# Optimization experiments

Measured on AMD Instinct MI355X. Metric: run time of the kernel, lower is better.

The kernel has to match this reference:

```python
import jax, jax.numpy as jnp
import numpy as np

B = 16384      # games
BS = 19        # board size
N2 = BS * BS   # 361
G = 8          # groups per board
S = 4          # stones per group
R = B * G      # total groups
K = R * S      # total stones
M = N2         # hash history length (H*W*history_factor)
I32MIN = np.iinfo(np.int32).min
I32MAX = np.iinfo(np.int32).max
NEG = jnp.float32(-1e9)


def setup_inputs() -> dict:
    key = jax.random.key(0)
    ks = jax.random.split(key, 10)
    logits = jax.random.normal(ks[0], (B, BS, BS), dtype=jnp.float32)
    legal_mask = jax.random.uniform(ks[1], (B, BS, BS)) < 0.7
    current_player = jax.random.randint(ks[2], (B,), 0, 2, dtype=jnp.int32)
    current_hash = jax.random.randint(ks[3], (B,), 0, I32MAX, dtype=jnp.int32)
    hash_history = jax.random.randint(ks[4], (B, M), 0, I32MAX, dtype=jnp.int32)
    move_count = jax.random.randint(ks[5], (B,), 0, M, dtype=jnp.int32)
    ZposT = jax.random.randint(ks[6], (3, N2), 0, I32MAX, dtype=jnp.int32)
    stone_global_index = jax.random.randint(ks[7], (K,), 0, N2, dtype=jnp.int32)
    stone_global_pointer = jnp.arange(R + 1, dtype=jnp.int32) * S          # CSR: stones per group
    group_global_pointer_per_board = jnp.arange(B + 1, dtype=jnp.int32) * G  # CSR: groups per board
    cap_idx = jax.random.randint(ks[8], (B, N2, 4), 0, G, dtype=jnp.int32)
    cap_on = jax.random.uniform(ks[9], (B, N2, 4)) < 0.05
    captured_group_local_index = jnp.where(cap_on, cap_idx, jnp.int32(-1))
    return {
        "logits": logits,
        "legal_mask": legal_mask,
        "current_player": current_player,
        "current_hash": current_hash,
        "hash_history": hash_history,
        "move_count": move_count,
        "ZposT": ZposT,
        "stone_global_index": stone_global_index,
        "stone_global_pointer": stone_global_pointer,
        "group_global_pointer_per_board": group_global_pointer_per_board,
        "captured_group_local_index": captured_group_local_index,
    }


def reference(logits, legal_mask, current_player, current_hash, hash_history,
              move_count, ZposT, stone_global_index, stone_global_pointer,
              group_global_pointer_per_board, captured_group_local_index):
    Bn, H, W = legal_mask.shape
    Rn = stone_global_pointer.shape[0] - 1
    Kn = stone_global_index.shape[0]
    z_empty, z_black, z_white = ZposT[0], ZposT[1], ZposT[2]

    # Placement delta: empty -> current player's stone, for every candidate point. (B, N2)
    placement_delta = z_empty[None, :] ^ jnp.where(
        (current_player == 0)[:, None], z_black[None, :], z_white[None, :])

    # Map each group -> board, each stone -> group (CSR expansion).
    groups_per_board = group_global_pointer_per_board[1:] - group_global_pointer_per_board[:-1]
    group_board = jnp.repeat(jnp.arange(Bn, dtype=jnp.int32), groups_per_board,
                             total_repeat_length=Rn)
    stones_per_group = stone_global_pointer[1:] - stone_global_pointer[:-1]
    group_for_stone = jnp.repeat(jnp.arange(Rn, dtype=jnp.int32), stones_per_group,
                                 total_repeat_length=Kn)
    stone_board = group_board[group_for_stone]

    # Per-stone removal delta: opponent stone -> empty.
    opp_for_stone = (1 - current_player)[stone_board]           # (K,)
    si = stone_global_index.astype(jnp.int32)
    z_opp = ZposT[1 + opp_for_stone, si]
    per_stone_delta = z_opp ^ z_empty[si]                        # (K,) int32

    # Segmented XOR reduction over each group's stones via XOR prefix scan.
    prefix = jax.lax.associative_scan(jnp.bitwise_xor, per_stone_delta)
    start = stone_global_pointer[:-1]
    end = stone_global_pointer[1:]
    end_val = prefix[jnp.clip(end - 1, 0)]
    start_val = jnp.where(start > 0, prefix[jnp.clip(start - 1, 0)], jnp.int32(0))
    group_xor = end_val ^ start_val                              # (R,) per-group removal delta

    # Gather capture deltas for up to 4 captured neighbor groups per candidate move.
    offs = group_global_pointer_per_board[:-1][:, None, None]    # (B,1,1)
    flat_ids = jnp.clip(captured_group_local_index, 0) + offs    # (B,N2,4)
    cap_vals = jnp.where(captured_group_local_index >= 0, group_xor[flat_ids], jnp.int32(0))
    capture_delta = cap_vals[..., 0] ^ cap_vals[..., 1] ^ cap_vals[..., 2] ^ cap_vals[..., 3]

    candidate = current_hash[:, None] ^ placement_delta ^ capture_delta  # (B, N2)

    # Super-ko repeat detection against hash history (mask, sort, searchsorted).
    Mh = hash_history.shape[1]
    valid = jnp.arange(Mh, dtype=jnp.int32)[None, :] < jnp.minimum(move_count, Mh)[:, None]
    masked_hist = jnp.where(valid, hash_history, jnp.int32(I32MIN))
    sorted_hist = jnp.sort(masked_hist, axis=1)
    idx = jnp.clip(
        jax.vmap(lambda h, c: jnp.searchsorted(h, c, side='right'))(sorted_hist, candidate) - 1,
        0)
    found = jnp.take_along_axis(sorted_hist, idx, axis=1)
    repeat = (found == candidate).reshape(Bn, H, W)

    final_mask = legal_mask & ~repeat
    return jnp.where(final_mask, logits, NEG)
```

## Files before the change

kernel.cpp:

```cpp
#include <hip/hip_runtime.h>
#include <stdint.h>

#define N2 361
#define BMW 1024u
#define EMPTY 0x80000000u
#define NEGV -998244352.0f

__global__ __launch_bounds__(256, 4) void go_repeat_mask_kernel(
    const float* __restrict__ logits,
    const void*  __restrict__ legal_raw,
    const int*   __restrict__ current_player,
    const int*   __restrict__ current_hash,
    const int*   __restrict__ hash_history,
    const int*   __restrict__ move_count,
    const int*   __restrict__ ZposT,
    const int*   __restrict__ stone_global_index,
    const int*   __restrict__ stone_global_pointer,
    const int*   __restrict__ group_global_pointer,
    const int4*  __restrict__ captured4,
    float*       __restrict__ out,
    int packed_bits)
{
    __shared__ unsigned s_bm[4 * BMW];

    const int tid  = threadIdx.x;
    const int wid  = tid >> 6;
    const int lane = tid & 63;
    const int b    = __builtin_amdgcn_readfirstlane(blockIdx.x * 4 + wid);
    unsigned* bm   = s_bm + wid * BMW;
    const size_t bbase = (size_t)b * N2;

    const int      cp  = current_player[b];
    const unsigned ch  = (unsigned)current_hash[b];
    int            cnt = move_count[b];
    cnt = cnt < 0 ? 0 : (cnt > N2 ? N2 : cnt);

    const int*  hist  = hash_history + bbase;
    const int4* hist4 = (const int4*)hist;
    const int4  ha    = hist4[lane];
    const int4  hb    = (lane < 26) ? hist4[64 + lane] : int4{0,0,0,0};
    const int   hc    = (lane == 26) ? hist[360] : 0;

    const unsigned* lwd = (const unsigned*)legal_raw;
    const unsigned dv0 = lwd[lane];
    const unsigned dv1 = (lane < 27) ? lwd[64 + lane] : 0u;

    int sp0 = 0, sp1 = 0;
    const int g0 = group_global_pointer[b];
    const int g1 = group_global_pointer[b + 1];
    if (lane < 32) {
        const int r = g0 + (lane >> 2);
        if (r < g1) { sp0 = stone_global_pointer[r]; sp1 = stone_global_pointer[r + 1]; }
    }

    int4  cap[6];
    float lg[6];
    unsigned zz[6];
    const int prow = (1 + cp) * N2;
    #pragma unroll
    for (int s = 0; s < 6; ++s) {
        const int n  = lane + 64 * s;
        const int nc = (n < N2) ? n : (N2 - 1);
        const size_t q = bbase + nc;
        cap[s] = captured4[q];
        lg[s]  = logits[q];
        zz[s]  = (unsigned)ZposT[nc] ^ (unsigned)ZposT[prow + nc];
    }

    auto classify = [](unsigned v) -> unsigned {
        unsigned f = 0;
        #pragma unroll
        for (int j = 0; j < 4; ++j) {
            const unsigned bv = (v >> (8 * j)) & 0xFFu;
            if (bv > 1u) f |= 1u;
            if (j != 0 && bv != 0u) f |= 2u;
        }
        const unsigned x = v & 0xFFFFu, y = v >> 16;
        if ((x && x != 0x3F80u) || (y && y != 0x3F80u)) f |= 4u;
        if (x == 0x3F80u) f |= 8u;
        return f;
    };
    unsigned fcl = classify(dv0);
    if (lane < 27) fcl |= classify(dv1);
    unsigned fa = 0;
    fa |= __ballot(fcl & 1u) ? 1u : 0u;
    fa |= __ballot(fcl & 2u) ? 2u : 0u;
    fa |= __ballot(fcl & 4u) ? 4u : 0u;
    fa |= __ballot(fcl & 8u) ? 8u : 0u;

    int fmt;
    if (packed_bits) fmt = 4;
    else if (!(fa & 1u)) fmt = 0;
    else if (!(fa & 4u)) fmt = (fa & 8u) ? 2 : 0;
    else fmt = 1;

    unsigned leg[6];
    #pragma unroll
    for (int s = 0; s < 6; ++s) {
        const int n = lane + 64 * s;
        const size_t q = bbase + ((n < N2) ? n : (N2 - 1));
        if (fmt == 0)      leg[s] = ((const unsigned*)legal_raw)[q];
        else if (fmt == 1) leg[s] = ((const uint8_t*)legal_raw)[q];
        else if (fmt == 2) leg[s] = ((const uint16_t*)legal_raw)[q];
        else               leg[s] = (((const uint8_t*)legal_raw)[q >> 3] >> (q & 7)) & 1u;
    }

    {
        uint4* t4 = (uint4*)bm;
        const uint4 z4 = {0u, 0u, 0u, 0u};
        #pragma unroll
        for (int i = 0; i < 4; ++i) t4[lane + 64 * i] = z4;
    }

    unsigned gx = 0u;
    if (lane < 32) {
        const int j = lane & 3;
        const int opprow = (2 - cp) * N2;
        for (int k = sp0 + j; k < sp1; k += 4) {
            const int si = stone_global_index[k];
            gx ^= (unsigned)ZposT[opprow + si] ^ (unsigned)ZposT[si];
        }
        gx ^= __shfl_xor(gx, 1);
        gx ^= __shfl_xor(gx, 2);
    }

    const int i0 = 4 * lane;
    const int i1 = 256 + 4 * lane;
    unsigned e0 = (i0 + 0 < cnt) ? (unsigned)ha.x : EMPTY;
    unsigned e1 = (i0 + 1 < cnt) ? (unsigned)ha.y : EMPTY;
    unsigned e2 = (i0 + 2 < cnt) ? (unsigned)ha.z : EMPTY;
    unsigned e3 = (i0 + 3 < cnt) ? (unsigned)ha.w : EMPTY;
    unsigned e4 = (lane < 26 && i1 + 0 < cnt) ? (unsigned)hb.x : EMPTY;
    unsigned e5 = (lane < 26 && i1 + 1 < cnt) ? (unsigned)hb.y : EMPTY;
    unsigned e6 = (lane < 26 && i1 + 2 < cnt) ? (unsigned)hb.z : EMPTY;
    unsigned e7 = (lane < 26 && i1 + 3 < cnt) ? (unsigned)hb.w : EMPTY;
    unsigned e8 = (lane == 26 && 360 < cnt)   ? (unsigned)hc   : EMPTY;

    asm volatile("s_waitcnt lgkmcnt(0)" ::: "memory");
    __builtin_amdgcn_sched_barrier(0);

    auto setbit = [&](unsigned v) {
        if (!(v & EMPTY)) atomicOr(&bm[(v >> 5) & (BMW - 1u)], 1u << (v & 31u));
    };
    setbit(e0); setbit(e1); setbit(e2); setbit(e3);
    setbit(e4); setbit(e5); setbit(e6); setbit(e7); setbit(e8);

    asm volatile("s_waitcnt lgkmcnt(0)" ::: "memory");
    __builtin_amdgcn_sched_barrier(0);

    unsigned cand[6], bw[6];
    #pragma unroll
    for (int s = 0; s < 6; ++s) {
        unsigned capd = 0u;
        const int4 c = cap[s];
        if (c.x >= 0) capd ^= (unsigned)__shfl((int)gx, (c.x & 7) * 4);
        if (c.y >= 0) capd ^= (unsigned)__shfl((int)gx, (c.y & 7) * 4);
        if (c.z >= 0) capd ^= (unsigned)__shfl((int)gx, (c.z & 7) * 4);
        if (c.w >= 0) capd ^= (unsigned)__shfl((int)gx, (c.w & 7) * 4);
        cand[s] = ch ^ zz[s] ^ capd;
        bw[s] = bm[(cand[s] >> 5) & (BMW - 1u)];
    }

    auto match9 = [&](unsigned c) -> bool {
        return (e0 == c) | (e1 == c) | (e2 == c) | (e3 == c) |
               (e4 == c) | (e5 == c) | (e6 == c) | (e7 == c) | (e8 == c);
    };

    #pragma unroll
    for (int s = 0; s < 6; ++s) {
        const int n = lane + 64 * s;
        const bool inr = n < N2;
        bool rep = false;
        unsigned long long mask = __ballot(inr && ((bw[s] >> (cand[s] & 31u)) & 1u));
        while (mask) {
            const int l = __ffsll((unsigned long long)mask) - 1;
            const unsigned c = (unsigned)__shfl((int)cand[s], l);
            const unsigned long long fm = __ballot(match9(c));
            if (lane == l) rep = (fm != 0ull);
            mask &= mask - 1;
        }
        if (inr) {
            const float v = (leg[s] && !rep) ? lg[s] : NEGV;
            __builtin_nontemporal_store(v, &out[bbase + n]);
        }
    }
}

extern "C" void kernel_launch(void* const* d_in, const int* in_sizes, int n_in,
                              void* d_out, int out_size, void* d_ws, size_t ws_size,
                              hipStream_t stream) {
    const float* logits  = (const float*)d_in[0];
    const void*  legal   = (const void*)d_in[1];
    const int*   cur_pl  = (const int*)d_in[2];
    const int*   cur_h   = (const int*)d_in[3];
    const int*   hist    = (const int*)d_in[4];
    const int*   mcount  = (const int*)d_in[5];
    const int*   zpos    = (const int*)d_in[6];
    const int*   sgi     = (const int*)d_in[7];
    const int*   sgp     = (const int*)d_in[8];
    const int*   ggp     = (const int*)d_in[9];
    const int4*  cap4    = (const int4*)d_in[10];
    float*       out     = (float*)d_out;

    const int B = in_sizes[2];
    const int packed = (in_sizes[1] != in_sizes[0]);

    go_repeat_mask_kernel<<<B / 4, 256, 0, stream>>>(
        logits, legal, cur_pl, cur_h, hist, mcount, zpos,
        sgi, sgp, ggp, cap4, out, packed);
}
```

Baseline: 221.7 us.

## Split fused kernel into group-hash, candidate, and mask kernels

Splits the single fused kernel into three launches. The first computes per-group XOR hashes and the legal-mask format flag once. The second writes candidate hashes to a workspace buffer, and the third builds the shared-memory bitmap filter and applies the mask. The bitmap shrinks to 512 words so eight boards fit per 512-thread block. The aim is to cut per-wave register and latency pressure from the serial stone loop and shuffles, at the cost of extra launches and a full round-trip of the candidate array through global memory. A fused fallback mode runs when the workspace is too small.

```diff
diff --git a/kernel.cpp b/kernel.cpp
--- a/kernel.cpp
+++ b/kernel.cpp
@@ -2,103 +2,175 @@
 #include <stdint.h>
 
 #define N2 361
-#define BMW 1024u
+#define BMW 512u
 #define EMPTY 0x80000000u
 #define NEGV -998244352.0f
 
-__global__ __launch_bounds__(256, 4) void go_repeat_mask_kernel(
+__global__ __launch_bounds__(256) void k_groups(
+    const int* __restrict__ current_player,
+    const int* __restrict__ ZposT,
+    const int* __restrict__ stone_global_index,
+    const int* __restrict__ stone_global_pointer,
+    unsigned*  __restrict__ gx_out,
+    const void* __restrict__ legal_raw,
+    unsigned*  __restrict__ fmt_out,
+    int packed_bits, int Rn)
+{
+    const int r = blockIdx.x * 256 + threadIdx.x;
+
+    if (blockIdx.x == 0 && threadIdx.x < 64) {
+        const int lane = threadIdx.x;
+        const unsigned* lwd = (const unsigned*)legal_raw;
+        const unsigned dv0 = lwd[lane];
+        const unsigned dv1 = (lane < 27) ? lwd[64 + lane] : 0u;
+        auto classify = [](unsigned v) -> unsigned {
+            unsigned f = 0;
+            #pragma unroll
+            for (int j = 0; j < 4; ++j) {
+                const unsigned bv = (v >> (8 * j)) & 0xFFu;
+                if (bv > 1u) f |= 1u;
+                if (j != 0 && bv != 0u) f |= 2u;
+            }
+            const unsigned x = v & 0xFFFFu, y = v >> 16;
+            if ((x && x != 0x3F80u) || (y && y != 0x3F80u)) f |= 4u;
+            if (x == 0x3F80u) f |= 8u;
+            return f;
+        };
+        unsigned fcl = classify(dv0);
+        if (lane < 27) fcl |= classify(dv1);
+        unsigned fa = 0;
+        fa |= __ballot(fcl & 1u) ? 1u : 0u;
+        fa |= __ballot(fcl & 2u) ? 2u : 0u;
+        fa |= __ballot(fcl & 4u) ? 4u : 0u;
+        fa |= __ballot(fcl & 8u) ? 8u : 0u;
+        unsigned fmt;
+        if (packed_bits) fmt = 4u;
+        else if (!(fa & 1u)) fmt = (fa & 2u) ? 1u : 0u;
+        else if (!(fa & 4u)) fmt = (fa & 8u) ? 2u : 0u;
+        else fmt = 1u;
+        if (lane == 0) fmt_out[0] = fmt;
+    }
+
+    if (r < Rn) {
+        const int sp0 = stone_global_pointer[r];
+        const int sp1 = stone_global_pointer[r + 1];
+        const int b   = r >> 3;
+        const int cp  = current_player[b];
+        const int opprow = (2 - cp) * N2;
+        unsigned x = 0u;
+        for (int k = sp0; k < sp1; ++k) {
+            const int si = stone_global_index[k];
+            x ^= (unsigned)ZposT[opprow + si] ^ (unsigned)ZposT[si];
+        }
+        gx_out[r] = x;
+    }
+}
+
+__device__ __forceinline__ unsigned sel8(uint4 a, uint4 b, unsigned i) {
+    const unsigned r01 = (i & 1u) ? a.y : a.x;
+    const unsigned r23 = (i & 1u) ? a.w : a.z;
+    const unsigned r45 = (i & 1u) ? b.y : b.x;
+    const unsigned r67 = (i & 1u) ? b.w : b.z;
+    const unsigned r03 = (i & 2u) ? r23 : r01;
+    const unsigned r47 = (i & 2u) ? r67 : r45;
+    return (i & 4u) ? r47 : r03;
+}
+
+__global__ __launch_bounds__(384) void k_cand(
+    const int* __restrict__ current_hash,
+    const int* __restrict__ current_player,
+    const int* __restrict__ ZposT,
+    const int4* __restrict__ captured4,
+    const unsigned* __restrict__ gx_ws,
+    unsigned* __restrict__ cand_out)
+{
+    const int b = blockIdx.x;
+    const int t = threadIdx.x;
+    if (t >= N2) return;
+    const unsigned ch = (unsigned)current_hash[b];
+    const int cp = current_player[b];
+    const uint4 ga = *(const uint4*)(gx_ws + b * 8);
+    const uint4 gb = *(const uint4*)(gx_ws + b * 8 + 4);
+    const size_t q = (size_t)b * N2 + t;
+    const int4 c = captured4[q];
+    unsigned capd = 0u;
+    if (c.x >= 0) capd ^= sel8(ga, gb, (unsigned)c.x & 7u);
+    if (c.y >= 0) capd ^= sel8(ga, gb, (unsigned)c.y & 7u);
+    if (c.z >= 0) capd ^= sel8(ga, gb, (unsigned)c.z & 7u);
+    if (c.w >= 0) capd ^= sel8(ga, gb, (unsigned)c.w & 7u);
+    const int prow = (1 + cp) * N2;
+    const unsigned zz = (unsigned)ZposT[t] ^ (unsigned)ZposT[prow + t];
+    cand_out[q] = ch ^ zz ^ capd;
+}
+
+template <int MODE>
+__global__ __launch_bounds__(512) void k_mask(
     const float* __restrict__ logits,
     const void*  __restrict__ legal_raw,
+    const int*   __restrict__ move_count,
+    const int*   __restrict__ hash_history,
+    const unsigned* __restrict__ cand_ws,
+    const unsigned* __restrict__ fmt_ws,
+    const int*   __restrict__ current_hash,
     const int*   __restrict__ current_player,
-    const int*   __restrict__ current_hash,
-    const int*   __restrict__ hash_history,
-    const int*   __restrict__ move_count,
     const int*   __restrict__ ZposT,
-    const int*   __restrict__ stone_global_index,
-    const int*   __restrict__ stone_global_pointer,
-    const int*   __restrict__ group_global_pointer,
     const int4*  __restrict__ captured4,
-    float*       __restrict__ out,
-    int packed_bits)
+    const unsigned* __restrict__ gx_ws,
+    float* __restrict__ out,
+    int Btot)
 {
-    __shared__ unsigned s_bm[4 * BMW];
-
+    __shared__ unsigned s_bm[8 * BMW];
     const int tid  = threadIdx.x;
     const int wid  = tid >> 6;
     const int lane = tid & 63;
-    const int b    = __builtin_amdgcn_readfirstlane(blockIdx.x * 4 + wid);
-    unsigned* bm   = s_bm + wid * BMW;
+    const int b    = __builtin_amdgcn_readfirstlane(blockIdx.x * 8 + wid);
+    if (b >= Btot) return;
+    unsigned* bm = s_bm + wid * BMW;
     const size_t bbase = (size_t)b * N2;
 
-    const int      cp  = current_player[b];
-    const unsigned ch  = (unsigned)current_hash[b];
-    int            cnt = move_count[b];
+    int cnt = move_count[b];
     cnt = cnt < 0 ? 0 : (cnt > N2 ? N2 : cnt);
+    const int fmt = (int)fmt_ws[0];
 
     const int*  hist  = hash_history + bbase;
     const int4* hist4 = (const int4*)hist;
     const int4  ha    = hist4[lane];
-    const int4  hb    = (lane < 26) ? hist4[64 + lane] : int4{0,0,0,0};
+    const int4  hb    = (lane < 26) ? hist4[64 + lane] : int4{0, 0, 0, 0};
     const int   hc    = (lane == 26) ? hist[360] : 0;
 
-    const unsigned* lwd = (const unsigned*)legal_raw;
-    const unsigned dv0 = lwd[lane];
-    const unsigned dv1 = (lane < 27) ? lwd[64 + lane] : 0u;
-
-    int sp0 = 0, sp1 = 0;
-    const int g0 = group_global_pointer[b];
-    const int g1 = group_global_pointer[b + 1];
-    if (lane < 32) {
-        const int r = g0 + (lane >> 2);
-        if (r < g1) { sp0 = stone_global_pointer[r]; sp1 = stone_global_pointer[r + 1]; }
-    }
-
-    int4  cap[6];
-    float lg[6];
-    unsigned zz[6];
-    const int prow = (1 + cp) * N2;
-    #pragma unroll
-    for (int s = 0; s < 6; ++s) {
-        const int n  = lane + 64 * s;
-        const int nc = (n < N2) ? n : (N2 - 1);
-        const size_t q = bbase + nc;
-        cap[s] = captured4[q];
-        lg[s]  = logits[q];
-        zz[s]  = (unsigned)ZposT[nc] ^ (unsigned)ZposT[prow + nc];
-    }
-
-    auto classify = [](unsigned v) -> unsigned {
-        unsigned f = 0;
+    unsigned cand[6];
+    if (MODE == 0) {
         #pragma unroll
-        for (int j = 0; j < 4; ++j) {
-            const unsigned bv = (v >> (8 * j)) & 0xFFu;
-            if (bv > 1u) f |= 1u;
-            if (j != 0 && bv != 0u) f |= 2u;
-        }
-        const unsigned x = v & 0xFFFFu, y = v >> 16;
-        if ((x && x != 0x3F80u) || (y && y != 0x3F80u)) f |= 4u;
-        if (x == 0x3F80u) f |= 8u;
-        return f;
-    };
-    unsigned fcl = classify(dv0);
-    if (lane < 27) fcl |= classify(dv1);
-    unsigned fa = 0;
-    fa |= __ballot(fcl & 1u) ? 1u : 0u;
-    fa |= __ballot(fcl & 2u) ? 2u : 0u;
-    fa |= __ballot(fcl & 4u) ? 4u : 0u;
-    fa |= __ballot(fcl & 8u) ? 8u : 0u;
-
-    int fmt;
-    if (packed_bits) fmt = 4;
-    else if (!(fa & 1u)) fmt = 0;
-    else if (!(fa & 4u)) fmt = (fa & 8u) ? 2 : 0;
-    else fmt = 1;
-
-    unsigned leg[6];
+        for (int s = 0; s < 6; ++s) {
+            const int n = lane + 64 * s;
+            cand[s] = cand_ws[bbase + ((n < N2) ? n : (N2 - 1))];
+        }
+    } else {
+        const unsigned ch = (unsigned)current_hash[b];
+        const int cp = current_player[b];
+        const int prow = (1 + cp) * N2;
+        const uint4 ga = *(const uint4*)(gx_ws + b * 8);
+        const uint4 gb2 = *(const uint4*)(gx_ws + b * 8 + 4);
+        #pragma unroll
+        for (int s = 0; s < 6; ++s) {
+            const int n  = lane + 64 * s;
+            const int nc = (n < N2) ? n : (N2 - 1);
+            const int4 c = captured4[bbase + nc];
+            unsigned capd = 0u;
+            if (c.x >= 0) capd ^= sel8(ga, gb2, (unsigned)c.x & 7u);
+            if (c.y >= 0) capd ^= sel8(ga, gb2, (unsigned)c.y & 7u);
+            if (c.z >= 0) capd ^= sel8(ga, gb2, (unsigned)c.z & 7u);
+            if (c.w >= 0) capd ^= sel8(ga, gb2, (unsigned)c.w & 7u);
+            cand[s] = ch ^ (unsigned)ZposT[nc] ^ (unsigned)ZposT[prow + nc] ^ capd;
+        }
+    }
+
+    float lg[6]; unsigned leg[6];
     #pragma unroll
     for (int s = 0; s < 6; ++s) {
         const int n = lane + 64 * s;
         const size_t q = bbase + ((n < N2) ? n : (N2 - 1));
+        lg[s] = logits[q];
         if (fmt == 0)      leg[s] = ((const unsigned*)legal_raw)[q];
         else if (fmt == 1) leg[s] = ((const uint8_t*)legal_raw)[q];
         else if (fmt == 2) leg[s] = ((const uint16_t*)legal_raw)[q];
@@ -108,33 +180,20 @@
     {
         uint4* t4 = (uint4*)bm;
         const uint4 z4 = {0u, 0u, 0u, 0u};
-        #pragma unroll
-        for (int i = 0; i < 4; ++i) t4[lane + 64 * i] = z4;
-    }
-
-    unsigned gx = 0u;
-    if (lane < 32) {
-        const int j = lane & 3;
-        const int opprow = (2 - cp) * N2;
-        for (int k = sp0 + j; k < sp1; k += 4) {
-            const int si = stone_global_index[k];
-            gx ^= (unsigned)ZposT[opprow + si] ^ (unsigned)ZposT[si];
-        }
-        gx ^= __shfl_xor(gx, 1);
-        gx ^= __shfl_xor(gx, 2);
-    }
-
-    const int i0 = 4 * lane;
-    const int i1 = 256 + 4 * lane;
-    unsigned e0 = (i0 + 0 < cnt) ? (unsigned)ha.x : EMPTY;
-    unsigned e1 = (i0 + 1 < cnt) ? (unsigned)ha.y : EMPTY;
-    unsigned e2 = (i0 + 2 < cnt) ? (unsigned)ha.z : EMPTY;
-    unsigned e3 = (i0 + 3 < cnt) ? (unsigned)ha.w : EMPTY;
-    unsigned e4 = (lane < 26 && i1 + 0 < cnt) ? (unsigned)hb.x : EMPTY;
-    unsigned e5 = (lane < 26 && i1 + 1 < cnt) ? (unsigned)hb.y : EMPTY;
-    unsigned e6 = (lane < 26 && i1 + 2 < cnt) ? (unsigned)hb.z : EMPTY;
-    unsigned e7 = (lane < 26 && i1 + 3 < cnt) ? (unsigned)hb.w : EMPTY;
-    unsigned e8 = (lane == 26 && 360 < cnt)   ? (unsigned)hc   : EMPTY;
+        t4[lane] = z4;
+        t4[64 + lane] = z4;
+    }
+
+    const int i0 = 4 * lane, i1 = 256 + 4 * lane;
+    const unsigned e0 = (i0 + 0 < cnt) ? (unsigned)ha.x : EMPTY;
+    const unsigned e1 = (i0 + 1 < cnt) ? (unsigned)ha.y : EMPTY;
+    const unsigned e2 = (i0 + 2 < cnt) ? (unsigned)ha.z : EMPTY;
+    const unsigned e3 = (i0 + 3 < cnt) ? (unsigned)ha.w : EMPTY;
+    const unsigned e4 = (lane < 26 && i1 + 0 < cnt) ? (unsigned)hb.x : EMPTY;
+    const unsigned e5 = (lane < 26 && i1 + 1 < cnt) ? (unsigned)hb.y : EMPTY;
+    const unsigned e6 = (lane < 26 && i1 + 2 < cnt) ? (unsigned)hb.z : EMPTY;
+    const unsigned e7 = (lane < 26 && i1 + 3 < cnt) ? (unsigned)hb.w : EMPTY;
+    const unsigned e8 = (lane == 26 && 360 < cnt)   ? (unsigned)hc   : EMPTY;
 
     asm volatile("s_waitcnt lgkmcnt(0)" ::: "memory");
     __builtin_amdgcn_sched_barrier(0);
@@ -148,18 +207,9 @@
     asm volatile("s_waitcnt lgkmcnt(0)" ::: "memory");
     __builtin_amdgcn_sched_barrier(0);
 
-    unsigned cand[6], bw[6];
+    unsigned bw[6];
     #pragma unroll
-    for (int s = 0; s < 6; ++s) {
-        unsigned capd = 0u;
-        const int4 c = cap[s];
-        if (c.x >= 0) capd ^= (unsigned)__shfl((int)gx, (c.x & 7) * 4);
-        if (c.y >= 0) capd ^= (unsigned)__shfl((int)gx, (c.y & 7) * 4);
-        if (c.z >= 0) capd ^= (unsigned)__shfl((int)gx, (c.z & 7) * 4);
-        if (c.w >= 0) capd ^= (unsigned)__shfl((int)gx, (c.w & 7) * 4);
-        cand[s] = ch ^ zz[s] ^ capd;
-        bw[s] = bm[(cand[s] >> 5) & (BMW - 1u)];
-    }
+    for (int s = 0; s < 6; ++s) bw[s] = bm[(cand[s] >> 5) & (BMW - 1u)];
 
     auto match9 = [&](unsigned c) -> bool {
         return (e0 == c) | (e1 == c) | (e2 == c) | (e3 == c) |
@@ -198,14 +248,33 @@
     const int*   zpos    = (const int*)d_in[6];
     const int*   sgi     = (const int*)d_in[7];
     const int*   sgp     = (const int*)d_in[8];
-    const int*   ggp     = (const int*)d_in[9];
     const int4*  cap4    = (const int4*)d_in[10];
     float*       out     = (float*)d_out;
 
-    const int B = in_sizes[2];
+    const int B  = in_sizes[2];
+    const int Rn = in_sizes[8] - 1;
     const int packed = (in_sizes[1] != in_sizes[0]);
 
-    go_repeat_mask_kernel<<<B / 4, 256, 0, stream>>>(
-        logits, legal, cur_pl, cur_h, hist, mcount, zpos,
-        sgi, sgp, ggp, cap4, out, packed);
-}
+    const size_t fmt_off  = (size_t)Rn * 4;
+    const size_t cand_off = ((fmt_off + 4 + 255) / 256) * 256;
+    const size_t need_full = cand_off + (size_t)B * N2 * 4;
+
+    unsigned* gx_ws   = (unsigned*)d_ws;
+    unsigned* fmt_ws  = (unsigned*)((char*)d_ws + fmt_off);
+    unsigned* cand_ws = (unsigned*)((char*)d_ws + cand_off);
+
+    k_groups<<<(Rn + 255) / 256, 256, 0, stream>>>(
+        cur_pl, zpos, sgi, sgp, gx_ws, legal, fmt_ws, packed, Rn);
+
+    const int mask_blocks = (B + 7) / 8;
+    if (ws_size >= need_full) {
+        k_cand<<<B, 384, 0, stream>>>(cur_h, cur_pl, zpos, cap4, gx_ws, cand_ws);
+        k_mask<0><<<mask_blocks, 512, 0, stream>>>(
+            logits, legal, mcount, hist, cand_ws, fmt_ws,
+            cur_h, cur_pl, zpos, cap4, gx_ws, out, B);
+    } else {
+        k_mask<1><<<mask_blocks, 512, 0, stream>>>(
+            logits, legal, mcount, hist, cand_ws, fmt_ws,
+            cur_h, cur_pl, zpos, cap4, gx_ws, out, B);
+    }
+}
```

New measurement: 229.5 us. 3.5% more time.
